# Performance work log

Measured on AMD Instinct MI355X. Metric: run time of the kernel, lower is better.

Reference implementation:

```python
import jax, jax.numpy as jnp
import numpy as np

S, B, E, H, M = 1024, 4, 1024, 16, 128  # seq, batch, embed, heads, model_dims (key width)
V = E // H                              # value_dims = 64
_WSCALE = 1.0 / np.sqrt(E)              # keep softmax logits O(1)


def _cplx(re, im):
    return jax.lax.complex(re, im)


def setup_inputs() -> dict:
    key = jax.random.key(0)
    ks = jax.random.split(key, 10)
    n = lambda k, shp: jax.random.normal(k, shp, dtype=jnp.float32)
    w = lambda k, shp: n(k, shp) * np.float32(_WSCALE / np.sqrt(2.0))
    return {
        "logits_re": n(ks[0], (S, B, E)),
        "logits_im": n(ks[1], (S, B, E)),
        "wq_re": w(ks[2], (H, M, E)), "wq_im": w(ks[3], (H, M, E)),
        "wk_re": w(ks[4], (H, M, E)), "wk_im": w(ks[5], (H, M, E)),
        "wv_re": w(ks[6], (H, V, E)), "wv_im": w(ks[7], (H, V, E)),
        "wo_re": w(ks[8], (E, E)),    "wo_im": w(ks[9], (E, E)),
    }


def reference(logits_re, logits_im, wq_re, wq_im, wk_re, wk_im,
              wv_re, wv_im, wo_re, wo_im):
    x = _cplx(logits_re, logits_im)          # (s, b, e) complex64
    wq = _cplx(wq_re, wq_im)                 # (h, m, e)
    wk = _cplx(wk_re, wk_im)
    wv = _cplx(wv_re, wv_im)                 # (h, v, e)
    wo = _cplx(wo_re, wo_im)                 # (e, e)

    q = jnp.einsum('hme,sbe->bhsm', wq, x)   # (b, h, s, m)
    k = jnp.einsum('hme,sbe->bhsm', wk, x)
    v = jnp.einsum('hve,sbe->bhsv', wv, x)   # (b, h, s, v)

    scores = jnp.einsum('bhsm,bhtm->bhst', q, k)         # complex, no conjugation (matches torch matmul)
    amp = jnp.abs(scores)                                # -> float32
    causal = jnp.triu(jnp.ones((S, S), dtype=bool), 1)   # True above diagonal -> masked
    amp = jnp.where(causal, -jnp.inf, amp) / jnp.sqrt(jnp.float32(M))
    attn = jax.nn.softmax(amp, axis=-1).astype(scores.dtype)  # cast back to complex64

    upd = jnp.einsum('bhst,bhtv->bhsv', attn, v)         # (b, h, s, v)
    upd = upd.transpose(2, 0, 1, 3).reshape(S, B, E)     # 's2 b (h v)'
    out = jnp.einsum('sbe,ef->sbf', upd, wo) + x         # residual
    # complex output returned as stacked (real, imag) float32 for harness compatibility
    return jnp.stack([out.real, out.imag])
```

## Files before the change

kernel.cpp:

```cpp
#include <hip/hip_runtime.h>
#include <math.h>

#define S_DIM 1024
#define B_DIM 4
#define E_DIM 1024
#define H_DIM 16
#define M_DIM 128
#define V_DIM 64

typedef __attribute__((ext_vector_type(8))) short short8;
typedef __attribute__((ext_vector_type(4))) float f32x4;
typedef __attribute__((ext_vector_type(4))) int int4v;

__device__ __forceinline__ unsigned short f2bf(float f) {
    union { float f; unsigned u; } v; v.f = f;
    unsigned r = v.u + 0x7FFFu + ((v.u >> 16) & 1u);
    return (unsigned short)(r >> 16);
}

__device__ __forceinline__ void async16(const unsigned short* g, unsigned short* l) {
    __builtin_amdgcn_global_load_lds(
        (const __attribute__((address_space(1))) void*)g,
        (__attribute__((address_space(3))) void*)l,
        16, 0, 0);
}

__global__ __launch_bounds__(256) void convert_all(
    const float* __restrict__ xre,  const float* __restrict__ xim,
    const float* __restrict__ wqre, const float* __restrict__ wqim,
    const float* __restrict__ wkre, const float* __restrict__ wkim,
    const float* __restrict__ wvre, const float* __restrict__ wvim,
    unsigned short* __restrict__ xbre, unsigned short* __restrict__ xbim,
    unsigned short* __restrict__ wbre, unsigned short* __restrict__ wbim)
{
    const int i = blockIdx.x * 256 + threadIdx.x;
    const float *re, *im;
    unsigned short *dr, *di;
    int j;
    if (i < 1048576)      { re = xre;  im = xim;  dr = xbre;               di = xbim;               j = i; }
    else if (i < 1572864) { re = wqre; im = wqim; dr = wbre;               di = wbim;               j = i - 1048576; }
    else if (i < 2097152) { re = wkre; im = wkim; dr = wbre + 2048 * 1024; di = wbim + 2048 * 1024; j = i - 1572864; }
    else                  { re = wvre; im = wvim; dr = wbre + 4096 * 1024; di = wbim + 4096 * 1024; j = i - 2097152; }
    float4 r = ((const float4*)re)[j];
    float4 m = ((const float4*)im)[j];
    ushort4 ro, mo;
    ro.x = f2bf(r.x); ro.y = f2bf(r.y); ro.z = f2bf(r.z); ro.w = f2bf(r.w);
    mo.x = f2bf(m.x); mo.y = f2bf(m.y); mo.z = f2bf(m.z); mo.w = f2bf(m.w);
    ((ushort4*)dr)[j] = ro;
    ((ushort4*)di)[j] = mo;
}

__global__ __launch_bounds__(256) void transpose_wo(
    const float* __restrict__ wore, const float* __restrict__ woim,
    unsigned short* __restrict__ wtre, unsigned short* __restrict__ wtim)
{
    __shared__ float tr[32][33], ti[32][33];
    const int bx = blockIdx.x * 32;
    const int by = blockIdx.y * 32;
    const int tx = threadIdx.x & 31, ty = threadIdx.x >> 5;
    for (int i = ty; i < 32; i += 8) {
        tr[i][tx] = wore[(bx + i) * E_DIM + by + tx];
        ti[i][tx] = woim[(bx + i) * E_DIM + by + tx];
    }
    __syncthreads();
    for (int i = ty; i < 32; i += 8) {
        wtre[(by + i) * E_DIM + bx + tx] = f2bf(tr[tx][i]);
        wtim[(by + i) * E_DIM + bx + tx] = f2bf(ti[tx][i]);
    }
}

__global__ __launch_bounds__(256) void vtrans(
    const unsigned short* __restrict__ vrp, const unsigned short* __restrict__ vip,
    unsigned short* __restrict__ vrt, unsigned short* __restrict__ vit)
{
    __shared__ unsigned short tl[2][64][66];
    const int tid = threadIdx.x;
    const int t0 = blockIdx.x * 64;
    const int bh = blockIdx.y;
    #pragma unroll
    for (int pl = 0; pl < 2; ++pl) {
        const unsigned short* src = pl ? vip : vrp;
        #pragma unroll
        for (int p = 0; p < 2; ++p) {
            const int row = p * 32 + (tid >> 3);
            const int col = (tid & 7) * 8;
            short8 d = *(const short8*)&src[((size_t)bh * S_DIM + t0 + row) * V_DIM + col];
            #pragma unroll
            for (int j = 0; j < 8; ++j) tl[pl][row][col + j] = (unsigned short)d[j];
        }
    }
    __syncthreads();
    #pragma unroll
    for (int pl = 0; pl < 2; ++pl) {
        unsigned short* dst = pl ? vit : vrt;
        #pragma unroll
        for (int p = 0; p < 2; ++p) {
            const int v = p * 32 + (tid >> 3);
            const int tc = (tid & 7) * 8;
            short8 d;
            #pragma unroll
            for (int j = 0; j < 8; ++j) d[j] = (short)tl[pl][tc + j][v];
            *(short8*)&dst[((size_t)bh * V_DIM + v) * S_DIM + t0 + tc] = d;
        }
    }
}

template<int MODE>
__global__ __launch_bounds__(256, 3) void cgemm(
    const unsigned short* __restrict__ Are, const unsigned short* __restrict__ Aim,
    const unsigned short* __restrict__ Bre, const unsigned short* __restrict__ Bim,
    unsigned short* __restrict__ qrp, unsigned short* __restrict__ qip,
    unsigned short* __restrict__ krp, unsigned short* __restrict__ kip,
    unsigned short* __restrict__ vrp, unsigned short* __restrict__ vip,
    const float* __restrict__ xre, const float* __restrict__ xim,
    float* __restrict__ out)
{
    __shared__ __align__(16) unsigned short lds[24576];
    const int tid  = threadIdx.x;
    const int wave = tid >> 6;
    const int lane = tid & 63;
    const int r0 = blockIdx.y * 128;
    const int j0 = blockIdx.x * 64;
    const int wm = (wave >> 1) * 64;
    const int wn = (wave & 1) * 32;

    f32x4 accre[4][2], accim[4][2];
    #pragma unroll
    for (int i = 0; i < 4; ++i)
        #pragma unroll
        for (int j = 0; j < 2; ++j) {
            accre[i][j] = (f32x4){0.f, 0.f, 0.f, 0.f};
            accim[i][j] = (f32x4){0.f, 0.f, 0.f, 0.f};
        }

    const int srow = lane >> 2;
    const int scol = ((lane & 3) ^ ((lane >> 3) & 3)) * 8;

    const int fr = lane & 15;
    const int xc = ((lane >> 4) ^ ((lane >> 1) & 3)) * 8;

    #define STAGE(sl, bb) { \
        const int kg = (sl) * 32; \
        unsigned short* b_ = &lds[(bb) * 12288]; \
        _Pragma("unroll") \
        for (int c = 0; c < 2; ++c) { \
            const int row0 = wave * 32 + c * 16; \
            const size_t g = (size_t)(r0 + row0 + srow) * E_DIM + kg + scol; \
            async16(Are + g, b_ + row0 * 32); \
            async16(Aim + g, b_ + 4096 + row0 * 32); \
        } \
        { \
            const int row0 = wave * 16; \
            const size_t g = (size_t)(j0 + row0 + srow) * E_DIM + kg + scol; \
            async16(Bre + g, b_ + 8192 + row0 * 32); \
            async16(Bim + g, b_ + 10240 + row0 * 32); \
        } }

    STAGE(0, 0)
    asm volatile("s_waitcnt vmcnt(0)" ::: "memory");
    __builtin_amdgcn_s_barrier();

    #pragma unroll 1
    for (int s = 0; s < 32; ++s) {
        if (s < 31) STAGE(s + 1, (s + 1) & 1)

        const unsigned short* buf = &lds[(s & 1) * 12288];
        short8 ar[4], ai[4], brr[2], bii[2];
        #pragma unroll
        for (int im = 0; im < 4; ++im) {
            const int ro = (wm + im * 16 + fr) * 32 + xc;
            ar[im] = *(const short8*)&buf[ro];
            ai[im] = *(const short8*)&buf[4096 + ro];
        }
        #pragma unroll
        for (int jn = 0; jn < 2; ++jn) {
            const int ro = (wn + jn * 16 + fr) * 32 + xc;
            brr[jn] = *(const short8*)&buf[8192 + ro];
            bii[jn] = *(const short8*)&buf[10240 + ro];
        }

        #pragma unroll
        for (int jn = 0; jn < 2; ++jn) {
            int4v t = *(int4v*)&bii[jn];
            t = t ^ (int)0x80008000;
            const short8 bin = *(short8*)&t;
            #pragma unroll
            for (int im = 0; im < 4; ++im) {
                accre[im][jn] = __builtin_amdgcn_mfma_f32_16x16x32_bf16(ar[im], brr[jn], accre[im][jn], 0, 0, 0);
                accre[im][jn] = __builtin_amdgcn_mfma_f32_16x16x32_bf16(ai[im], bin,     accre[im][jn], 0, 0, 0);
                accim[im][jn] = __builtin_amdgcn_mfma_f32_16x16x32_bf16(ar[im], bii[jn], accim[im][jn], 0, 0, 0);
                accim[im][jn] = __builtin_amdgcn_mfma_f32_16x16x32_bf16(ai[im], brr[jn], accim[im][jn], 0, 0, 0);
            }
        }

        if (s < 31) {
            asm volatile("s_waitcnt vmcnt(0)" ::: "memory");
            __builtin_amdgcn_s_barrier();
        }
    }
    #undef STAGE

    #pragma unroll
    for (int im = 0; im < 4; ++im) {
        #pragma unroll
        for (int reg = 0; reg < 4; ++reg) {
            const int r = r0 + wm + im * 16 + (lane >> 4) * 4 + reg;
            #pragma unroll
            for (int jn = 0; jn < 2; ++jn) {
                const int j = j0 + wn + jn * 16 + fr;
                const float vr = accre[im][jn][reg];
                const float vi = accim[im][jn][reg];
                if (MODE == 0) {
                    const int s = r >> 2, b = r & 3;
                    if (j < 2048) {
                        const int h = j >> 7, m = j & 127;
                        const size_t off = ((size_t)(b * H_DIM + h) * S_DIM + s) * M_DIM + m;
                        qrp[off] = f2bf(vr); qip[off] = f2bf(vi);
                    } else if (j < 4096) {
                        const int jl = j - 2048, h = jl >> 7, m = jl & 127;
                        const size_t off = ((size_t)(b * H_DIM + h) * S_DIM + s) * M_DIM + m;
                        krp[off] = f2bf(vr); kip[off] = f2bf(vi);
                    } else {
                        const int jl = j - 4096, h = jl >> 6, vv = jl & 63;
                        const size_t off = ((size_t)(b * H_DIM + h) * S_DIM + s) * V_DIM + vv;
                        vrp[off] = f2bf(vr); vip[off] = f2bf(vi);
                    }
                } else {
                    const int idx = r * E_DIM + j;
                    out[idx] = vr + xre[idx];
                    out[S_DIM * B_DIM * E_DIM + idx] = vi + xim[idx];
                }
            }
        }
    }
}

__global__ __launch_bounds__(256, 2) void attn_mfma(
    const unsigned short* __restrict__ qr, const unsigned short* __restrict__ qi,
    const unsigned short* __restrict__ kr, const unsigned short* __restrict__ ki,
    const unsigned short* __restrict__ vrt, const unsigned short* __restrict__ vit,
    unsigned short* __restrict__ updre, unsigned short* __restrict__ updim)
{
    __shared__ __align__(16) unsigned short Ks[2][64][136];
    __shared__ __align__(16) unsigned short Vs[2][64][72];
    __shared__ __align__(16) unsigned short Ps[4][16][80];

    const int tid  = threadIdx.x;
    const int wave = tid >> 6;
    const int lane = tid & 63;
    const int qt = (int)gridDim.x - 1 - blockIdx.x;
    const int bh = blockIdx.y;
    const int q0 = qt * 64;
    const size_t base_qk = (size_t)bh * S_DIM * M_DIM;
    const size_t base_v  = (size_t)bh * V_DIM * S_DIM;

    const int fr = lane & 15;
    const int fg = lane >> 4;
    const int fk = fg * 8;

    const int krow = tid >> 4, kcol = (tid & 15) * 8;
    const int vrow = tid >> 3, vcol = (tid & 7) * 8;

    #pragma unroll
    for (int pl = 0; pl < 2; ++pl) {
        const unsigned short* src = pl ? qi : qr;
        #pragma unroll
        for (int p = 0; p < 4; ++p)
            *(short8*)&Ks[pl][p * 16 + krow][kcol] =
                *(const short8*)&src[base_qk + (size_t)(q0 + p * 16 + krow) * M_DIM + kcol];
    }
    __syncthreads();
    short8 Bqr[4], Bqi[4];
    {
        const int qrow = wave * 16 + fr;
        #pragma unroll
        for (int ks = 0; ks < 4; ++ks) {
            Bqr[ks] = *(const short8*)&Ks[0][qrow][ks * 32 + fk];
            Bqi[ks] = *(const short8*)&Ks[1][qrow][ks * 32 + fk];
        }
    }

    f32x4 Ore[4], Oim[4];
    #pragma unroll
    for (int vt = 0; vt < 4; ++vt) {
        Ore[vt] = (f32x4){0.f, 0.f, 0.f, 0.f};
        Oim[vt] = (f32x4){0.f, 0.f, 0.f, 0.f};
    }
    float mrun = -INFINITY, lrun = 0.f;

    const float scale = 0.088388347648318447f;
    const int qglob = q0 + wave * 16 + fr;

    short8 pk[2][4], pv[2][2];
    #pragma unroll
    for (int pl = 0; pl < 2; ++pl) {
        const unsigned short* src = pl ? ki : kr;
        #pragma unroll
        for (int p = 0; p < 4; ++p)
            pk[pl][p] = *(const short8*)&src[base_qk + (size_t)(p * 16 + krow) * M_DIM + kcol];
    }
    #pragma unroll
    for (int pl = 0; pl < 2; ++pl) {
        const unsigned short* src = pl ? vit : vrt;
        #pragma unroll
        for (int p = 0; p < 2; ++p)
            pv[pl][p] = *(const short8*)&src[base_v + (size_t)(p * 32 + vrow) * S_DIM + vcol];
    }

    for (int t0 = 0; t0 <= q0; t0 += 64) {
        __syncthreads();
        #pragma unroll
        for (int pl = 0; pl < 2; ++pl) {
            #pragma unroll
            for (int p = 0; p < 4; ++p)
                *(short8*)&Ks[pl][p * 16 + krow][kcol] = pk[pl][p];
            #pragma unroll
            for (int p = 0; p < 2; ++p)
                *(short8*)&Vs[pl][p * 32 + vrow][vcol] = pv[pl][p];
        }
        __syncthreads();

        if (t0 + 64 <= q0) {
            const int tn = t0 + 64;
            #pragma unroll
            for (int pl = 0; pl < 2; ++pl) {
                const unsigned short* src = pl ? ki : kr;
                #pragma unroll
                for (int p = 0; p < 4; ++p)
                    pk[pl][p] = *(const short8*)&src[base_qk + (size_t)(tn + p * 16 + krow) * M_DIM + kcol];
            }
            #pragma unroll
            for (int pl = 0; pl < 2; ++pl) {
                const unsigned short* src = pl ? vit : vrt;
                #pragma unroll
                for (int p = 0; p < 2; ++p)
                    pv[pl][p] = *(const short8*)&src[base_v + (size_t)(p * 32 + vrow) * S_DIM + tn + vcol];
            }
        }

        f32x4 Sre[4], Sim[4];
        __builtin_amdgcn_s_setprio(1);
        #pragma unroll
        for (int tt = 0; tt < 4; ++tt) {
            Sre[tt] = (f32x4){0.f, 0.f, 0.f, 0.f};
            Sim[tt] = (f32x4){0.f, 0.f, 0.f, 0.f};
            const int trow = tt * 16 + fr;
            #pragma unroll
            for (int ks = 0; ks < 4; ++ks) {
                const short8 Akr = *(const short8*)&Ks[0][trow][ks * 32 + fk];
                const short8 Aki = *(const short8*)&Ks[1][trow][ks * 32 + fk];
                int4v t = *(int4v*)&Aki;
                t = t ^ (int)0x80008000;
                const short8 Akin = *(short8*)&t;
                Sre[tt] = __builtin_amdgcn_mfma_f32_16x16x32_bf16(Akr,  Bqr[ks], Sre[tt], 0, 0, 0);
                Sre[tt] = __builtin_amdgcn_mfma_f32_16x16x32_bf16(Akin, Bqi[ks], Sre[tt], 0, 0, 0);
                Sim[tt] = __builtin_amdgcn_mfma_f32_16x16x32_bf16(Akr,  Bqi[ks], Sim[tt], 0, 0, 0);
                Sim[tt] = __builtin_amdgcn_mfma_f32_16x16x32_bf16(Aki,  Bqr[ks], Sim[tt], 0, 0, 0);
            }
        }
        __builtin_amdgcn_s_setprio(0);

        float amp[4][4];
        float rowmax = -INFINITY;
        #pragma unroll
        for (int tt = 0; tt < 4; ++tt) {
            #pragma unroll
            for (int r = 0; r < 4; ++r) {
                const int tg = t0 + tt * 16 + fg * 4 + r;
                const float re = Sre[tt][r], im = Sim[tt][r];
                const float a = sqrtf(re * re + im * im) * scale;
                const float av = (tg > qglob) ? -INFINITY : a;
                amp[tt][r] = av;
                rowmax = fmaxf(rowmax, av);
            }
        }
        rowmax = fmaxf(rowmax, __shfl_xor(rowmax, 16));
        rowmax = fmaxf(rowmax, __shfl_xor(rowmax, 32));
        const float nm = fmaxf(mrun, rowmax);
        const float alpha = __expf(mrun - nm);
        mrun = nm;
        float psum = 0.f;
        #pragma unroll
        for (int tt = 0; tt < 4; ++tt) {
            #pragma unroll
            for (int r = 0; r < 4; ++r) {
                const float p = __expf(amp[tt][r] - nm);
                psum += p;
                Ps[wave][fr][tt * 16 + fg * 4 + r] = f2bf(p);
            }
        }
        psum += __shfl_xor(psum, 16);
        psum += __shfl_xor(psum, 32);
        lrun = lrun * alpha + psum;

        #pragma unroll
        for (int vt = 0; vt < 4; ++vt)
            #pragma unroll
            for (int r = 0; r < 4; ++r) { Ore[vt][r] *= alpha; Oim[vt][r] *= alpha; }

        const short8 Bp0 = *(const short8*)&Ps[wave][fr][fk];
        const short8 Bp1 = *(const short8*)&Ps[wave][fr][32 + fk];
        __builtin_amdgcn_s_setprio(1);
        #pragma unroll
        for (int vt = 0; vt < 4; ++vt) {
            const int vr2 = vt * 16 + fr;
            const short8 Ar0 = *(const short8*)&Vs[0][vr2][fk];
            const short8 Ar1 = *(const short8*)&Vs[0][vr2][32 + fk];
            const short8 Ai0 = *(const short8*)&Vs[1][vr2][fk];
            const short8 Ai1 = *(const short8*)&Vs[1][vr2][32 + fk];
            Ore[vt] = __builtin_amdgcn_mfma_f32_16x16x32_bf16(Ar0, Bp0, Ore[vt], 0, 0, 0);
            Ore[vt] = __builtin_amdgcn_mfma_f32_16x16x32_bf16(Ar1, Bp1, Ore[vt], 0, 0, 0);
            Oim[vt] = __builtin_amdgcn_mfma_f32_16x16x32_bf16(Ai0, Bp0, Oim[vt], 0, 0, 0);
            Oim[vt] = __builtin_amdgcn_mfma_f32_16x16x32_bf16(Ai1, Bp1, Oim[vt], 0, 0, 0);
        }
        __builtin_amdgcn_s_setprio(0);
    }

    const int b = bh >> 4, h = bh & 15;
    const float inv = 1.0f / lrun;
    const size_t base = ((size_t)(qglob * B_DIM + b)) * E_DIM + h * V_DIM;
    #pragma unroll
    for (int vt = 0; vt < 4; ++vt) {
        ushort4 pr, pi;
        pr.x = f2bf(Ore[vt][0] * inv); pr.y = f2bf(Ore[vt][1] * inv);
        pr.z = f2bf(Ore[vt][2] * inv); pr.w = f2bf(Ore[vt][3] * inv);
        pi.x = f2bf(Oim[vt][0] * inv); pi.y = f2bf(Oim[vt][1] * inv);
        pi.z = f2bf(Oim[vt][2] * inv); pi.w = f2bf(Oim[vt][3] * inv);
        *(ushort4*)&updre[base + vt * 16 + fg * 4] = pr;
        *(ushort4*)&updim[base + vt * 16 + fg * 4] = pi;
    }
}

extern "C" void kernel_launch(void* const* d_in, const int* in_sizes, int n_in,
                              void* d_out, int out_size, void* d_ws, size_t ws_size,
                              hipStream_t stream) {
    const float* xre  = (const float*)d_in[0];
    const float* xim  = (const float*)d_in[1];
    const float* wqre = (const float*)d_in[2];
    const float* wqim = (const float*)d_in[3];
    const float* wkre = (const float*)d_in[4];
    const float* wkim = (const float*)d_in[5];
    const float* wvre = (const float*)d_in[6];
    const float* wvim = (const float*)d_in[7];
    const float* wore = (const float*)d_in[8];
    const float* woim = (const float*)d_in[9];
    float* out = (float*)d_out;

    char* p = (char*)d_ws;
    const size_t QK = (size_t)B_DIM * H_DIM * S_DIM * M_DIM;
    const size_t VS = (size_t)B_DIM * H_DIM * S_DIM * V_DIM;
    const size_t SBE = (size_t)S_DIM * B_DIM * E_DIM;
    unsigned short* qrw = (unsigned short*)p;  p += QK * 2;
    unsigned short* qiw = (unsigned short*)p;  p += QK * 2;
    unsigned short* krw = (unsigned short*)p;  p += QK * 2;
    unsigned short* kiw = (unsigned short*)p;  p += QK * 2;
    unsigned short* vrw = (unsigned short*)p;  p += VS * 2;
    unsigned short* viw = (unsigned short*)p;  p += VS * 2;
    unsigned short* vrt = (unsigned short*)p;  p += VS * 2;
    unsigned short* vit = (unsigned short*)p;  p += VS * 2;
    unsigned short* updre = (unsigned short*)p; p += SBE * 2;
    unsigned short* updim = (unsigned short*)p; p += SBE * 2;
    unsigned short* xbre  = (unsigned short*)p; p += SBE * 2;
    unsigned short* xbim  = (unsigned short*)p; p += SBE * 2;
    unsigned short* wbre  = (unsigned short*)p; p += (size_t)5120 * E_DIM * 2;
    unsigned short* wbim  = (unsigned short*)p; p += (size_t)5120 * E_DIM * 2;
    unsigned short* wtre  = (unsigned short*)p; p += (size_t)E_DIM * E_DIM * 2;
    unsigned short* wtim  = (unsigned short*)p; p += (size_t)E_DIM * E_DIM * 2;

    convert_all<<<9216, 256, 0, stream>>>(xre, xim, wqre, wqim, wkre, wkim, wvre, wvim,
                                          xbre, xbim, wbre, wbim);
    transpose_wo<<<dim3(32, 32), 256, 0, stream>>>(wore, woim, wtre, wtim);

    cgemm<0><<<dim3(80, 32), 256, 0, stream>>>(xbre, xbim, wbre, wbim,
                                               qrw, qiw, krw, kiw, vrw, viw,
                                               nullptr, nullptr, nullptr);
    vtrans<<<dim3(16, 64), 256, 0, stream>>>(vrw, viw, vrt, vit);
    attn_mfma<<<dim3(16, 64), 256, 0, stream>>>(qrw, qiw, krw, kiw, vrt, vit, updre, updim);
    cgemm<1><<<dim3(16, 32), 256, 0, stream>>>(updre, updim, wtre, wtim,
                                               nullptr, nullptr, nullptr, nullptr, nullptr, nullptr,
                                               xre, xim, out);
}
```

Before: 476.4 us.

## Enlarge complex GEMM tiles to 128x128 using 32x32x16 MFMA instructions

Both complex GEMMs (QKV projection and output projection) now use 128x128 block tiles instead of 128x64, with each wave computing a 64x64 sub-tile through 32x32x16 bf16 MFMAs in place of 16x16x32. The grid is reordered so the row dimension runs along blockIdx.x, and LDS grows to hold the wider B tile. The aim is more arithmetic per LDS and global byte and fewer fragment loads. The cost is more accumulator registers, occupancy lowered to 2 blocks per CU, and fewer blocks for the smaller output GEMM (256 blocks).

```diff
diff --git a/kernel.cpp b/kernel.cpp
--- a/kernel.cpp
+++ b/kernel.cpp
@@ -10,6 +10,7 @@
 
 typedef __attribute__((ext_vector_type(8))) short short8;
 typedef __attribute__((ext_vector_type(4))) float f32x4;
+typedef __attribute__((ext_vector_type(16))) float f32x16;
 typedef __attribute__((ext_vector_type(4))) int int4v;
 
 __device__ __forceinline__ unsigned short f2bf(float f) {
@@ -106,7 +107,7 @@
 }
 
 template<int MODE>
-__global__ __launch_bounds__(256, 3) void cgemm(
+__global__ __launch_bounds__(256, 2) void cgemm(
     const unsigned short* __restrict__ Are, const unsigned short* __restrict__ Aim,
     const unsigned short* __restrict__ Bre, const unsigned short* __restrict__ Bim,
     unsigned short* __restrict__ qrp, unsigned short* __restrict__ qip,
@@ -115,46 +116,47 @@
     const float* __restrict__ xre, const float* __restrict__ xim,
     float* __restrict__ out)
 {
-    __shared__ __align__(16) unsigned short lds[24576];
+    __shared__ __align__(16) unsigned short lds[32768];
     const int tid  = threadIdx.x;
     const int wave = tid >> 6;
     const int lane = tid & 63;
-    const int r0 = blockIdx.y * 128;
-    const int j0 = blockIdx.x * 64;
+    const int r0 = blockIdx.x * 128;
+    const int j0 = blockIdx.y * 128;
     const int wm = (wave >> 1) * 64;
-    const int wn = (wave & 1) * 32;
-
-    f32x4 accre[4][2], accim[4][2];
-    #pragma unroll
-    for (int i = 0; i < 4; ++i)
+    const int wn = (wave & 1) * 64;
+
+    f32x16 accre[2][2], accim[2][2];
+    #pragma unroll
+    for (int i = 0; i < 2; ++i)
         #pragma unroll
         for (int j = 0; j < 2; ++j) {
-            accre[i][j] = (f32x4){0.f, 0.f, 0.f, 0.f};
-            accim[i][j] = (f32x4){0.f, 0.f, 0.f, 0.f};
-        }
-
-    const int srow = lane >> 2;
-    const int scol = ((lane & 3) ^ ((lane >> 3) & 3)) * 8;
-
-    const int fr = lane & 15;
-    const int xc = ((lane >> 4) ^ ((lane >> 1) & 3)) * 8;
+            #pragma unroll
+            for (int e = 0; e < 16; ++e) { accre[i][j][e] = 0.f; accim[i][j][e] = 0.f; }
+        }
+
+    const int sr   = tid >> 2;
+    const int sc   = (tid & 3) * 8;
+    const int scol = ((tid & 3) ^ ((tid >> 3) & 3)) * 8;
+
+    const int l31 = lane & 31;
+    const int l5  = lane >> 5;
+    const int lxk = (lane >> 1) & 3;
 
     #define STAGE(sl, bb) { \
         const int kg = (sl) * 32; \
-        unsigned short* b_ = &lds[(bb) * 12288]; \
-        _Pragma("unroll") \
-        for (int c = 0; c < 2; ++c) { \
-            const int row0 = wave * 32 + c * 16; \
-            const size_t g = (size_t)(r0 + row0 + srow) * E_DIM + kg + scol; \
-            async16(Are + g, b_ + row0 * 32); \
-            async16(Aim + g, b_ + 4096 + row0 * 32); \
-        } \
-        { \
-            const int row0 = wave * 16; \
-            const size_t g = (size_t)(j0 + row0 + srow) * E_DIM + kg + scol; \
-            async16(Bre + g, b_ + 8192 + row0 * 32); \
-            async16(Bim + g, b_ + 10240 + row0 * 32); \
-        } }
+        unsigned short* b_ = &lds[(bb) * 16384]; \
+        const size_t ga0 = (size_t)(r0 + sr) * E_DIM + kg + scol; \
+        const size_t ga1 = (size_t)(r0 + 64 + sr) * E_DIM + kg + scol; \
+        const size_t gb0 = (size_t)(j0 + sr) * E_DIM + kg + scol; \
+        const size_t gb1 = (size_t)(j0 + 64 + sr) * E_DIM + kg + scol; \
+        async16(Are + ga0, b_ + sr * 32 + sc); \
+        async16(Are + ga1, b_ + (64 + sr) * 32 + sc); \
+        async16(Aim + ga0, b_ + 4096 + sr * 32 + sc); \
+        async16(Aim + ga1, b_ + 4096 + (64 + sr) * 32 + sc); \
+        async16(Bre + gb0, b_ + 8192 + sr * 32 + sc); \
+        async16(Bre + gb1, b_ + 8192 + (64 + sr) * 32 + sc); \
+        async16(Bim + gb0, b_ + 12288 + sr * 32 + sc); \
+        async16(Bim + gb1, b_ + 12288 + (64 + sr) * 32 + sc); }
 
     STAGE(0, 0)
     asm volatile("s_waitcnt vmcnt(0)" ::: "memory");
@@ -164,32 +166,36 @@
     for (int s = 0; s < 32; ++s) {
         if (s < 31) STAGE(s + 1, (s + 1) & 1)
 
-        const unsigned short* buf = &lds[(s & 1) * 12288];
-        short8 ar[4], ai[4], brr[2], bii[2];
-        #pragma unroll
-        for (int im = 0; im < 4; ++im) {
-            const int ro = (wm + im * 16 + fr) * 32 + xc;
-            ar[im] = *(const short8*)&buf[ro];
-            ai[im] = *(const short8*)&buf[4096 + ro];
-        }
-        #pragma unroll
-        for (int jn = 0; jn < 2; ++jn) {
-            const int ro = (wn + jn * 16 + fr) * 32 + xc;
-            brr[jn] = *(const short8*)&buf[8192 + ro];
-            bii[jn] = *(const short8*)&buf[10240 + ro];
-        }
-
-        #pragma unroll
-        for (int jn = 0; jn < 2; ++jn) {
-            int4v t = *(int4v*)&bii[jn];
-            t = t ^ (int)0x80008000;
-            const short8 bin = *(short8*)&t;
-            #pragma unroll
-            for (int im = 0; im < 4; ++im) {
-                accre[im][jn] = __builtin_amdgcn_mfma_f32_16x16x32_bf16(ar[im], brr[jn], accre[im][jn], 0, 0, 0);
-                accre[im][jn] = __builtin_amdgcn_mfma_f32_16x16x32_bf16(ai[im], bin,     accre[im][jn], 0, 0, 0);
-                accim[im][jn] = __builtin_amdgcn_mfma_f32_16x16x32_bf16(ar[im], bii[jn], accim[im][jn], 0, 0, 0);
-                accim[im][jn] = __builtin_amdgcn_mfma_f32_16x16x32_bf16(ai[im], brr[jn], accim[im][jn], 0, 0, 0);
+        const unsigned short* buf = &lds[(s & 1) * 16384];
+
+        #pragma unroll
+        for (int kk = 0; kk < 2; ++kk) {
+            const int ck = ((kk * 2 + l5) ^ lxk) * 8;
+            short8 ar[2], ai[2], br[2], bi[2];
+            #pragma unroll
+            for (int mt = 0; mt < 2; ++mt) {
+                const int ro = (wm + mt * 32 + l31) * 32 + ck;
+                ar[mt] = *(const short8*)&buf[ro];
+                ai[mt] = *(const short8*)&buf[4096 + ro];
+            }
+            #pragma unroll
+            for (int nt = 0; nt < 2; ++nt) {
+                const int ro = (wn + nt * 32 + l31) * 32 + ck;
+                br[nt] = *(const short8*)&buf[8192 + ro];
+                bi[nt] = *(const short8*)&buf[12288 + ro];
+            }
+            #pragma unroll
+            for (int nt = 0; nt < 2; ++nt) {
+                int4v t = *(int4v*)&bi[nt];
+                t = t ^ (int)0x80008000;
+                const short8 bin = *(short8*)&t;
+                #pragma unroll
+                for (int mt = 0; mt < 2; ++mt) {
+                    accre[mt][nt] = __builtin_amdgcn_mfma_f32_32x32x16_bf16(ar[mt], br[nt], accre[mt][nt], 0, 0, 0);
+                    accre[mt][nt] = __builtin_amdgcn_mfma_f32_32x32x16_bf16(ai[mt], bin,    accre[mt][nt], 0, 0, 0);
+                    accim[mt][nt] = __builtin_amdgcn_mfma_f32_32x32x16_bf16(ar[mt], bi[nt], accim[mt][nt], 0, 0, 0);
+                    accim[mt][nt] = __builtin_amdgcn_mfma_f32_32x32x16_bf16(ai[mt], br[nt], accim[mt][nt], 0, 0, 0);
+                }
             }
         }
 
@@ -201,15 +207,15 @@
     #undef STAGE
 
     #pragma unroll
-    for (int im = 0; im < 4; ++im) {
-        #pragma unroll
-        for (int reg = 0; reg < 4; ++reg) {
-            const int r = r0 + wm + im * 16 + (lane >> 4) * 4 + reg;
-            #pragma unroll
-            for (int jn = 0; jn < 2; ++jn) {
-                const int j = j0 + wn + jn * 16 + fr;
-                const float vr = accre[im][jn][reg];
-                const float vi = accim[im][jn][reg];
+    for (int mt = 0; mt < 2; ++mt) {
+        #pragma unroll
+        for (int nt = 0; nt < 2; ++nt) {
+            #pragma unroll
+            for (int reg = 0; reg < 16; ++reg) {
+                const int r = r0 + wm + mt * 32 + (reg & 3) + 8 * (reg >> 2) + 4 * l5;
+                const int j = j0 + wn + nt * 32 + l31;
+                const float vr = accre[mt][nt][reg];
+                const float vi = accim[mt][nt][reg];
                 if (MODE == 0) {
                     const int s = r >> 2, b = r & 3;
                     if (j < 2048) {
@@ -471,12 +477,12 @@
                                           xbre, xbim, wbre, wbim);
     transpose_wo<<<dim3(32, 32), 256, 0, stream>>>(wore, woim, wtre, wtim);
 
-    cgemm<0><<<dim3(80, 32), 256, 0, stream>>>(xbre, xbim, wbre, wbim,
+    cgemm<0><<<dim3(32, 40), 256, 0, stream>>>(xbre, xbim, wbre, wbim,
                                                qrw, qiw, krw, kiw, vrw, viw,
                                                nullptr, nullptr, nullptr);
     vtrans<<<dim3(16, 64), 256, 0, stream>>>(vrw, viw, vrt, vit);
     attn_mfma<<<dim3(16, 64), 256, 0, stream>>>(qrw, qiw, krw, kiw, vrt, vit, updre, updim);
-    cgemm<1><<<dim3(16, 32), 256, 0, stream>>>(updre, updim, wtre, wtim,
-                                               nullptr, nullptr, nullptr, nullptr, nullptr, nullptr,
-                                               xre, xim, out);
-}
+    cgemm<1><<<dim3(32, 8), 256, 0, stream>>>(updre, updim, wtre, wtim,
+                                              nullptr, nullptr, nullptr, nullptr, nullptr, nullptr,
+                                              xre, xim, out);
+}
```

Result: slower. 494.2 us (+3.7%).
